# Performance work log

Hardware: AMD Instinct MI355X
Metric: run time of the kernel (lower is better)

## Reference

```python
import jax, jax.numpy as jnp
import numpy as np
import math

D_MODEL = 1024
D_STATE = 16
D_CONV = 4
EXPAND = 2
D_INNER = EXPAND * D_MODEL  # 2048
DT_RANK = 64
B_SZ = 2
L_SEQ = 1024


def setup_inputs() -> dict:
    key = jax.random.key(0)
    ks = jax.random.split(key, 10)
    x = jax.random.normal(ks[0], (B_SZ, L_SEQ, D_MODEL), dtype=jnp.float32)
    in_proj_w = jax.random.normal(ks[1], (2 * D_INNER, D_MODEL), dtype=jnp.float32) * (1.0 / math.sqrt(D_MODEL))
    conv_w = jax.random.normal(ks[2], (D_INNER, 1, D_CONV), dtype=jnp.float32) * (1.0 / math.sqrt(D_CONV))
    conv_b = jax.random.normal(ks[3], (D_INNER,), dtype=jnp.float32) * 0.01
    x_proj_w = jax.random.normal(ks[4], (DT_RANK + 2 * D_STATE, D_INNER), dtype=jnp.float32) * (1.0 / math.sqrt(D_INNER))
    dt_init_std = DT_RANK ** (-0.5)
    dt_proj_w = jax.random.uniform(ks[5], (D_INNER, DT_RANK), dtype=jnp.float32, minval=-dt_init_std, maxval=dt_init_std)
    dt = jnp.exp(jax.random.uniform(ks[6], (D_INNER,), dtype=jnp.float32) * (math.log(0.1) - math.log(0.001)) + math.log(0.001))
    dt = jnp.clip(dt, 1e-4, None)
    dt_proj_b = dt + jnp.log(-jnp.expm1(-dt))
    A_log = jnp.log(jnp.tile(jnp.arange(1, D_STATE + 1, dtype=jnp.float32)[None, :], (D_INNER, 1)))
    D = jnp.ones((D_INNER,), dtype=jnp.float32)
    out_proj_w = jax.random.normal(ks[7], (D_MODEL, D_INNER), dtype=jnp.float32) * (1.0 / math.sqrt(D_INNER))
    return {"x": x, "in_proj_w": in_proj_w, "conv_w": conv_w, "conv_b": conv_b,
            "x_proj_w": x_proj_w, "dt_proj_w": dt_proj_w, "dt_proj_b": dt_proj_b,
            "A_log": A_log, "D": D, "out_proj_w": out_proj_w}


def _mamba_forward(x, in_proj_w, conv_w, conv_b, x_proj_w, dt_proj_w, dt_proj_b, A_log, D, out_proj_w):
    B, L, _ = x.shape
    # input projection -> x, z each [B, L, Di]
    xz = jnp.einsum('bld,ed->ble', x, in_proj_w)
    xs, z = jnp.split(xz, 2, axis=-1)
    # causal depthwise conv along L (torch pads K-1 both sides then trims -> left pad only)
    xc = jnp.transpose(xs, (0, 2, 1))  # [B, Di, L]
    xc = jax.lax.conv_general_dilated(
        xc, conv_w, window_strides=(1,), padding=[(D_CONV - 1, 0)],
        feature_group_count=D_INNER, dimension_numbers=('NCH', 'OIH', 'NCH'))
    xc = xc + conv_b[None, :, None]
    xs = jnp.transpose(xc, (0, 2, 1))  # [B, L, Di]
    xs = jax.nn.silu(xs)
    # SSM parameters
    A = -jnp.exp(A_log)  # [Di, N]
    dbc = jnp.einsum('bld,ed->ble', xs, x_proj_w)
    delta_r = dbc[..., :DT_RANK]
    Bm = dbc[..., DT_RANK:DT_RANK + D_STATE]       # [B, L, N]
    Cm = dbc[..., DT_RANK + D_STATE:]              # [B, L, N]
    delta = jnp.einsum('blr,dr->bld', delta_r, dt_proj_w)
    delta = jax.nn.softplus(delta + dt_proj_b)     # [B, L, Di]
    # selective scan: h_t = exp(delta*A)*h_{t-1} + delta*B*x
    dA = jnp.exp(delta[..., None] * A)                          # [B, L, Di, N]
    dBx = (delta * xs)[..., None] * Bm[:, :, None, :]           # [B, L, Di, N]
    dA_t = jnp.moveaxis(dA, 1, 0)    # [L, B, Di, N]
    dBx_t = jnp.moveaxis(dBx, 1, 0)
    C_t = jnp.moveaxis(Cm, 1, 0)     # [L, B, N]
    h0 = jnp.zeros((B, D_INNER, D_STATE), dtype=xs.dtype)

    def step(h, inp):
        da, bx, c = inp
        h = da * h + bx
        y = jnp.einsum('bdn,bn->bd', h, c)
        return h, y

    _, ys = jax.lax.scan(step, h0, (dA_t, dBx_t, C_t))
    y = jnp.moveaxis(ys, 0, 1)       # [B, L, Di]
    y = y + D * xs
    # gating and output projection
    out = y * jax.nn.silu(z)
    return jnp.einsum('bld,od->blo', out, out_proj_w)


def reference(x, in_proj_w, conv_w, conv_b, x_proj_w, dt_proj_w, dt_proj_b, A_log, D, out_proj_w):
    return _mamba_forward(x, in_proj_w, conv_w, conv_b, x_proj_w, dt_proj_w, dt_proj_b, A_log, D, out_proj_w)
```

## Files before the change

kernel.cpp:

```cpp
#include <hip/hip_runtime.h>
#include <hip/hip_bf16.h>

typedef __attribute__((ext_vector_type(8))) short short8;
typedef __attribute__((ext_vector_type(4))) float f32x4;
typedef __hip_bfloat16 bf16;

#define D_MODEL 1024
#define D_INNER 2048
#define DT_RANK 64
#define D_STATE 16
#define B_SZ 2
#define L_SEQ 1024
#define NSEG 32
#define SL 32

__device__ __forceinline__ float b2f(bf16 x){ return __bfloat162float(x); }
__device__ __forceinline__ bf16  f2b(float x){ return __float2bfloat16(x); }

__device__ __forceinline__ void cvt_store8(bf16* dst, const float* s){
  union { short8 v; bf16 e[8]; } u;
  #pragma unroll
  for (int i = 0; i < 8; i++) u.e[i] = f2b(s[i]);
  *(short8*)dst = u.v;
}

__device__ __forceinline__ void gl_lds16(const bf16* g, bf16* l){
  __builtin_amdgcn_global_load_lds((const __attribute__((address_space(1))) unsigned int*)g,
                                   (__attribute__((address_space(3))) unsigned int*)l, 16, 0, 0);
}

__global__ __launch_bounds__(256) void cvt5_k(const float* s0, bf16* d0, int c0,
                                              const float* s1, bf16* d1, int c1,
                                              const float* s2, bf16* d2, int c2,
                                              const float* s3, bf16* d3, int c3,
                                              const float* s4, bf16* d4, int c4)
{
  int i = blockIdx.x * 256 + threadIdx.x;
  const float* s; bf16* d; int off;
  if      (i < c0) { s = s0; d = d0; off = i; }
  else if (i < c1) { s = s1; d = d1; off = i - c0; }
  else if (i < c2) { s = s2; d = d2; off = i - c1; }
  else if (i < c3) { s = s3; d = d3; off = i - c2; }
  else if (i < c4) { s = s4; d = d4; off = i - c3; }
  else return;
  float b[8];
  *(float4*)&b[0] = *(const float4*)(s + (size_t)off * 8);
  *(float4*)&b[4] = *(const float4*)(s + (size_t)off * 8 + 4);
  cvt_store8(d + (size_t)off * 8, b);
}

template<int MODE, int JT>
__global__ __launch_bounds__(256) void gemm_glds(const bf16* __restrict__ A,
                                                 const bf16* __restrict__ B,
                                                 void* __restrict__ Cout,
                                                 int M, int N, int K)
{
  constexpr int BN = JT * 32;
  constexpr int BI = BN / 64;
  __shared__ bf16 As[128 * 32];
  __shared__ bf16 Bs[BN * 32];

  const int gx = gridDim.x;
  const int nwg = gx * gridDim.y;
  const int flat = blockIdx.y * gx + blockIdx.x;
  const int swz = (flat & 7) * (nwg >> 3) + (flat >> 3);
  const int bm = (swz / gx) * 128, bn = (swz % gx) * BN;

  const int tid  = threadIdx.x;
  const int lane = tid & 63, wave = tid >> 6;
  const int wm = (wave & 1) * 64, wn = (wave >> 1) * (JT * 16);
  const int r = lane & 15, q = lane >> 4;

  const bf16* asrc[2];
  #pragma unroll
  for (int i = 0; i < 2; i++) {
    int c = i * 256 + tid;
    asrc[i] = A + (size_t)(bm + (c >> 2)) * K + (c & 3) * 8;
  }
  const bf16* bsrc[BI];
  #pragma unroll
  for (int i = 0; i < BI; i++) {
    int c = i * 256 + tid;
    bsrc[i] = B + (size_t)(bn + (c >> 2)) * K + (c & 3) * 8;
  }

  f32x4 acc[4][JT];
  #pragma unroll
  for (int i = 0; i < 4; i++)
    #pragma unroll
    for (int j = 0; j < JT; j++) acc[i][j] = (f32x4){0.f,0.f,0.f,0.f};

  for (int k0 = 0; k0 < K; k0 += 32) {
    #pragma unroll
    for (int i = 0; i < 2; i++)
      gl_lds16(asrc[i] + k0, &As[(i * 256 + tid) * 8]);
    #pragma unroll
    for (int i = 0; i < BI; i++)
      gl_lds16(bsrc[i] + k0, &Bs[(i * 256 + tid) * 8]);
    __syncthreads();
    short8 af[4], bfr[JT];
    #pragma unroll
    for (int i = 0; i < 4; i++)  af[i]  = *(const short8*)&As[(wm + i*16 + r) * 32 + q*8];
    #pragma unroll
    for (int j = 0; j < JT; j++) bfr[j] = *(const short8*)&Bs[(wn + j*16 + r) * 32 + q*8];
    #pragma unroll
    for (int j = 0; j < JT; j++)
      #pragma unroll
      for (int i = 0; i < 4; i++)
        acc[i][j] = __builtin_amdgcn_mfma_f32_16x16x32_bf16(af[i], bfr[j], acc[i][j], 0, 0, 0);
    __syncthreads();
  }

  #pragma unroll
  for (int i = 0; i < 4; i++)
    #pragma unroll
    for (int j = 0; j < JT; j++)
      #pragma unroll
      for (int t = 0; t < 4; t++) {
        int row = bm + wm + i*16 + q*4 + t;
        int col = bn + wn + j*16 + r;
        float v = acc[i][j][t];
        if (MODE == 0) ((float*)Cout)[(size_t)row * N + col] = v;
        else           ((bf16*)Cout)[(size_t)row * N + col] = f2b(v);
      }
}

__global__ __launch_bounds__(256) void gemm_dt(const bf16* __restrict__ A,
                                               const bf16* __restrict__ W,
                                               float* __restrict__ Cout,
                                               const float* __restrict__ bias,
                                               int M, int N)
{
  __shared__ __align__(16) float stg[4][16][68];
  const int lane = threadIdx.x & 63, wave = threadIdx.x >> 6;
  const int ntg  = N >> 6;
  const int task = blockIdx.x * 4 + wave;
  const int mt   = task / ntg;
  const int ng   = task - mt * ntg;
  const int r = lane & 15, q = lane >> 4;

  const bf16* pa = A + (size_t)(mt*16 + r) * DT_RANK + q*8;
  short8 a0 = *(const short8*)pa;
  short8 a1 = *(const short8*)(pa + 32);

  #pragma unroll
  for (int j = 0; j < 4; j++) {
    const bf16* pb = W + (size_t)(ng*64 + j*16 + r) * DT_RANK + q*8;
    short8 b0 = *(const short8*)pb;
    short8 b1 = *(const short8*)(pb + 32);
    f32x4 c = {0.f,0.f,0.f,0.f};
    c = __builtin_amdgcn_mfma_f32_16x16x32_bf16(a0, b0, c, 0, 0, 0);
    c = __builtin_amdgcn_mfma_f32_16x16x32_bf16(a1, b1, c, 0, 0, 0);
    float bv = bias[ng*64 + j*16 + r];
    #pragma unroll
    for (int t = 0; t < 4; t++) {
      float xv = c[t] + bv;
      float sp = (xv > 20.f) ? xv : log1pf(__expf(xv));
      stg[wave][q*4 + t][j*16 + r] = sp;
    }
  }
  {
    int row = lane >> 2, q4 = lane & 3;
    const float* src = &stg[wave][row][q4 * 16];
    float4 w0 = *(const float4*)(src);
    float4 w1 = *(const float4*)(src + 4);
    float4 w2 = *(const float4*)(src + 8);
    float4 w3 = *(const float4*)(src + 12);
    float* gdst = Cout + (size_t)(mt*16 + row) * N + ng*64 + q4*16;
    *(float4*)(gdst)      = w0;
    *(float4*)(gdst + 4)  = w1;
    *(float4*)(gdst + 8)  = w2;
    *(float4*)(gdst + 12) = w3;
  }
}

__global__ __launch_bounds__(256) void gemm_xproj(const bf16* __restrict__ A,
                                                  const bf16* __restrict__ W,
                                                  float* __restrict__ dbc,
                                                  bf16* __restrict__ dr)
{
  const int K = D_INNER;
  const int lane = threadIdx.x & 63, wave = threadIdx.x >> 6;
  const int mt = blockIdx.y * 4 + wave;
  const int nt = blockIdx.x;
  const int r = lane & 15, q = lane >> 4;
  const bf16* pa = A + (size_t)(mt*16 + r) * K + q*8;
  const bf16* pb = W + (size_t)(nt*16 + r) * K + q*8;
  f32x4 a0 = {0.f,0.f,0.f,0.f}, a1 = a0, a2 = a0, a3 = a0;
  for (int k0 = 0; k0 < K; k0 += 128) {
    short8 x0 = *(const short8*)(pa + k0);
    short8 w0 = *(const short8*)(pb + k0);
    short8 x1 = *(const short8*)(pa + k0 + 32);
    short8 w1 = *(const short8*)(pb + k0 + 32);
    short8 x2 = *(const short8*)(pa + k0 + 64);
    short8 w2 = *(const short8*)(pb + k0 + 64);
    short8 x3 = *(const short8*)(pa + k0 + 96);
    short8 w3 = *(const short8*)(pb + k0 + 96);
    a0 = __builtin_amdgcn_mfma_f32_16x16x32_bf16(x0, w0, a0, 0, 0, 0);
    a1 = __builtin_amdgcn_mfma_f32_16x16x32_bf16(x1, w1, a1, 0, 0, 0);
    a2 = __builtin_amdgcn_mfma_f32_16x16x32_bf16(x2, w2, a2, 0, 0, 0);
    a3 = __builtin_amdgcn_mfma_f32_16x16x32_bf16(x3, w3, a3, 0, 0, 0);
  }
  f32x4 acc = (a0 + a1) + (a2 + a3);
  #pragma unroll
  for (int t = 0; t < 4; t++) {
    int row = mt*16 + q*4 + t;
    int col = nt*16 + r;
    dbc[(size_t)row * 96 + col] = acc[t];
    if (col < DT_RANK) dr[(size_t)row * DT_RANK + col] = f2b(acc[t]);
  }
}

__global__ __launch_bounds__(256) void conv_silu_k(const bf16* __restrict__ xz,
                                                   const float* __restrict__ cw,
                                                   const float* __restrict__ cb,
                                                   bf16* __restrict__ xs_b)
{
  int idx = blockIdx.x * 256 + threadIdx.x;
  int dg = idx & (D_INNER/8 - 1);
  int bl = idx >> 8;
  int l  = bl & (L_SEQ - 1);
  int d0 = dg * 8;
  const float4* cw4 = (const float4*)cw;
  float4 w[8];
  #pragma unroll
  for (int i = 0; i < 8; i++) w[i] = cw4[d0 + i];
  float acc[8];
  #pragma unroll
  for (int i = 0; i < 8; i++) acc[i] = cb[d0 + i];
  #pragma unroll
  for (int j = 0; j < 4; ++j) {
    int lp = l - 3 + j;
    if (lp >= 0) {
      short8 v = *(const short8*)(xz + (size_t)(bl - 3 + j) * (2*D_INNER) + d0);
      #pragma unroll
      for (int i = 0; i < 8; i++)
        acc[i] += ((const float*)&w[i])[j] * b2f(((const bf16*)&v)[i]);
    }
  }
  float o[8];
  #pragma unroll
  for (int i = 0; i < 8; i++) o[i] = acc[i] / (1.f + __expf(-acc[i]));
  cvt_store8(xs_b + (size_t)idx * 8, o);
}

__device__ __forceinline__ bool an_is_int(const float* An){
  bool f = true;
  #pragma unroll
  for (int n = 0; n < 16; n++) f = f & (fabsf(An[n] + (float)(n+1)) < 1e-3f);
  return f;
}

__global__ __launch_bounds__(256) void scan_pass1(const float* __restrict__ delta,
                                                  const bf16* __restrict__ xs,
                                                  const float* __restrict__ dbc,
                                                  const float* __restrict__ A_log,
                                                  float* __restrict__ hseg,
                                                  float* __restrict__ Stot)
{
  __shared__ float bcs[SL][32];
  const int d   = blockIdx.x * 256 + threadIdx.x;
  const int seg = blockIdx.y, b = blockIdx.z;
  for (int i = threadIdx.x; i < SL*32; i += 256) {
    int l = i >> 5, c = i & 31;
    bcs[l][c] = dbc[((size_t)b*L_SEQ + seg*SL + l)*96 + DT_RANK + c];
  }
  __syncthreads();
  float An[16], h[16];
  #pragma unroll
  for (int n = 0; n < 16; n++) { An[n] = -__expf(A_log[d*16 + n]); h[n] = 0.f; }
  float S = 0.f;
  if (an_is_int(An)) {
    for (int li = 0; li < SL; ++li) {
      size_t bl = (size_t)b * L_SEQ + seg*SL + li;
      float dv = delta[bl*D_INNER + d];
      float xv = b2f(xs[bl*D_INNER + d]);
      S += dv;
      float dx = dv * xv;
      float q = __expf(-dv), w = 1.f;
      #pragma unroll
      for (int n = 0; n < 16; n++) {
        w *= q;
        h[n] = w * h[n] + dx * bcs[li][n];
      }
    }
  } else {
    for (int li = 0; li < SL; ++li) {
      size_t bl = (size_t)b * L_SEQ + seg*SL + li;
      float dv = delta[bl*D_INNER + d];
      float xv = b2f(xs[bl*D_INNER + d]);
      S += dv;
      float dx = dv * xv;
      #pragma unroll
      for (int n = 0; n < 16; n++)
        h[n] = __expf(dv * An[n]) * h[n] + dx * bcs[li][n];
    }
  }
  float* hp = hseg + (((size_t)seg*B_SZ + b)*D_INNER + d) * 16;
  #pragma unroll
  for (int n = 0; n < 16; n++) hp[n] = h[n];
  Stot[((size_t)seg*B_SZ + b)*D_INNER + d] = S;
}

__global__ __launch_bounds__(256) void scan_combine(const float* __restrict__ Stot,
                                                    float* __restrict__ hseg,
                                                    const float* __restrict__ A_log)
{
  int idx = blockIdx.x * 256 + threadIdx.x;
  int n = idx & 15;
  int d = (idx >> 4) & (D_INNER - 1);
  int b = idx >> 15;
  float An = -__expf(A_log[d*16 + n]);
  float H = 0.f;
  for (int s = 0; s < NSEG; s++) {
    size_t base = ((size_t)s*B_SZ + b)*D_INNER + d;
    float St   = Stot[base];
    float hloc = hseg[base*16 + n];
    hseg[base*16 + n] = H;
    H = __expf(An*St)*H + hloc;
  }
}

__global__ __launch_bounds__(256) void scan_pass3(const float* __restrict__ delta,
                                                  const bf16* __restrict__ xs,
                                                  const float* __restrict__ dbc,
                                                  const float* __restrict__ A_log,
                                                  const float* __restrict__ hseg,
                                                  const bf16* __restrict__ xz,
                                                  const float* __restrict__ Dw,
                                                  bf16* __restrict__ outin)
{
  __shared__ float bcs[SL][32];
  const int d   = blockIdx.x * 256 + threadIdx.x;
  const int seg = blockIdx.y, b = blockIdx.z;
  for (int i = threadIdx.x; i < SL*32; i += 256) {
    int l = i >> 5, c = i & 31;
    bcs[l][c] = dbc[((size_t)b*L_SEQ + seg*SL + l)*96 + DT_RANK + c];
  }
  __syncthreads();
  float An[16], h[16];
  const float* hp = hseg + (((size_t)seg*B_SZ + b)*D_INNER + d) * 16;
  #pragma unroll
  for (int n = 0; n < 16; n++) { An[n] = -__expf(A_log[d*16 + n]); h[n] = hp[n]; }
  const float Dv = Dw[d];
  if (an_is_int(An)) {
    for (int li = 0; li < SL; ++li) {
      size_t bl = (size_t)b * L_SEQ + seg*SL + li;
      float dv = delta[bl*D_INNER + d];
      float xv = b2f(xs[bl*D_INNER + d]);
      float dx = dv * xv;
      float q = __expf(-dv), w = 1.f;
      float y = 0.f;
      #pragma unroll
      for (int n = 0; n < 16; n++) {
        w *= q;
        h[n] = w * h[n] + dx * bcs[li][n];
        y   += h[n] * bcs[li][16 + n];
      }
      y += Dv * xv;
      float z = b2f(xz[bl*(size_t)(2*D_INNER) + D_INNER + d]);
      float g = z / (1.f + __expf(-z));
      outin[bl*D_INNER + d] = f2b(y * g);
    }
  } else {
    for (int li = 0; li < SL; ++li) {
      size_t bl = (size_t)b * L_SEQ + seg*SL + li;
      float dv = delta[bl*D_INNER + d];
      float xv = b2f(xs[bl*D_INNER + d]);
      float dx = dv * xv;
      float y = 0.f;
      #pragma unroll
      for (int n = 0; n < 16; n++) {
        h[n] = __expf(dv * An[n]) * h[n] + dx * bcs[li][n];
        y   += h[n] * bcs[li][16 + n];
      }
      y += Dv * xv;
      float z = b2f(xz[bl*(size_t)(2*D_INNER) + D_INNER + d]);
      float g = z / (1.f + __expf(-z));
      outin[bl*D_INNER + d] = f2b(y * g);
    }
  }
}

extern "C" void kernel_launch(void* const* d_in, const int* in_sizes, int n_in,
                              void* d_out, int out_size, void* d_ws, size_t ws_size,
                              hipStream_t stream)
{
  const float* x      = (const float*)d_in[0];
  const float* in_w   = (const float*)d_in[1];
  const float* conv_w = (const float*)d_in[2];
  const float* conv_b = (const float*)d_in[3];
  const float* xp_w   = (const float*)d_in[4];
  const float* dt_w   = (const float*)d_in[5];
  const float* dt_b   = (const float*)d_in[6];
  const float* A_log  = (const float*)d_in[7];
  const float* Dw     = (const float*)d_in[8];
  const float* out_w  = (const float*)d_in[9];
  float* out = (float*)d_out;

  char* p = (char*)d_ws;
  bf16*  xz    = (bf16*)p;  p += (size_t)B_SZ*L_SEQ*2*D_INNER*2;
  bf16*  xs_b  = (bf16*)p;  p += (size_t)B_SZ*L_SEQ*D_INNER*2;
  float* dbc   = (float*)p; p += (size_t)B_SZ*L_SEQ*96*4;
  bf16*  dr    = (bf16*)p;  p += (size_t)B_SZ*L_SEQ*DT_RANK*2;
  float* delta = (float*)p; p += (size_t)B_SZ*L_SEQ*D_INNER*4;
  float* Stot  = (float*)p; p += (size_t)NSEG*B_SZ*D_INNER*4;
  bf16*  outin = (bf16*)p;  p += (size_t)B_SZ*L_SEQ*D_INNER*2;
  bf16*  xp_wb = (bf16*)p;  p += (size_t)(DT_RANK+2*D_STATE)*D_INNER*2;
  bf16*  dt_wb = (bf16*)p;  p += (size_t)D_INNER*DT_RANK*2;
  bf16*  ow_b  = (bf16*)p;  p += (size_t)D_MODEL*D_INNER*2;
  char* u = p;
  bf16*  xb    = (bf16*)u;
  bf16*  in_wb = (bf16*)(u + (size_t)B_SZ*L_SEQ*D_MODEL*2);
  float* hseg  = (float*)u;
  p += (size_t)B_SZ*L_SEQ*(D_MODEL + 2*D_INNER)*2;

  const int M = B_SZ * L_SEQ;

  cvt5_k<<<4256, 256, 0, stream>>>(x, xb, 262144,
                                   in_w, in_wb, 786432,
                                   xp_w, xp_wb, 811008,
                                   dt_w, dt_wb, 827392,
                                   out_w, ow_b, 1089536);
  gemm_glds<2,2><<<dim3(2*D_INNER/64, M/128), 256, 0, stream>>>(xb, in_wb, xz, M, 2*D_INNER, D_MODEL);
  conv_silu_k<<<(M*D_INNER/8)/256, 256, 0, stream>>>(xz, conv_w, conv_b, xs_b);
  gemm_xproj<<<dim3(6, M/64), 256, 0, stream>>>(xs_b, xp_wb, dbc, dr);
  gemm_dt<<<(M/16)*(D_INNER/64)/4, 256, 0, stream>>>(dr, dt_wb, delta, dt_b, M, D_INNER);
  scan_pass1<<<dim3(D_INNER/256, NSEG, B_SZ), 256, 0, stream>>>(delta, xs_b, dbc, A_log, hseg, Stot);
  scan_combine<<<(B_SZ*D_INNER*16)/256, 256, 0, stream>>>(Stot, hseg, A_log);
  scan_pass3<<<dim3(D_INNER/256, NSEG, B_SZ), 256, 0, stream>>>(delta, xs_b, dbc, A_log, hseg, xz, Dw, outin);
  gemm_glds<0,2><<<dim3(D_MODEL/64, M/128), 256, 0, stream>>>(outin, ow_b, out, M, D_MODEL, D_INNER);
}
```

Before: 255.3 us.

## Fuse conv, projections and scan stages into one cooperative persistent kernel

Replaces six separate launches (conv+silu, x_proj GEMM, dt GEMM with softplus, scan pass1, segment combine, scan pass3) with a single cooperative kernel of 512 blocks separated by grid-wide syncs. The intent is to eliminate inter-kernel launch gaps and tail effects between these short stages. In exchange each stage runs with a fixed 512-block grid, some stages leave blocks idle, and grid.sync adds its own barrier cost; shared memory is reused across stages.

New measurement: 592.1 us. +131.9%, slower.

```diff
diff --git a/kernel.cpp b/kernel.cpp
--- a/kernel.cpp
+++ b/kernel.cpp
@@ -1,5 +1,8 @@
 #include <hip/hip_runtime.h>
 #include <hip/hip_bf16.h>
+#include <hip/hip_cooperative_groups.h>
+
+namespace cg = cooperative_groups;
 
 typedef __attribute__((ext_vector_type(8))) short short8;
 typedef __attribute__((ext_vector_type(4))) float f32x4;
@@ -125,125 +128,6 @@
       }
 }
 
-__global__ __launch_bounds__(256) void gemm_dt(const bf16* __restrict__ A,
-                                               const bf16* __restrict__ W,
-                                               float* __restrict__ Cout,
-                                               const float* __restrict__ bias,
-                                               int M, int N)
-{
-  __shared__ __align__(16) float stg[4][16][68];
-  const int lane = threadIdx.x & 63, wave = threadIdx.x >> 6;
-  const int ntg  = N >> 6;
-  const int task = blockIdx.x * 4 + wave;
-  const int mt   = task / ntg;
-  const int ng   = task - mt * ntg;
-  const int r = lane & 15, q = lane >> 4;
-
-  const bf16* pa = A + (size_t)(mt*16 + r) * DT_RANK + q*8;
-  short8 a0 = *(const short8*)pa;
-  short8 a1 = *(const short8*)(pa + 32);
-
-  #pragma unroll
-  for (int j = 0; j < 4; j++) {
-    const bf16* pb = W + (size_t)(ng*64 + j*16 + r) * DT_RANK + q*8;
-    short8 b0 = *(const short8*)pb;
-    short8 b1 = *(const short8*)(pb + 32);
-    f32x4 c = {0.f,0.f,0.f,0.f};
-    c = __builtin_amdgcn_mfma_f32_16x16x32_bf16(a0, b0, c, 0, 0, 0);
-    c = __builtin_amdgcn_mfma_f32_16x16x32_bf16(a1, b1, c, 0, 0, 0);
-    float bv = bias[ng*64 + j*16 + r];
-    #pragma unroll
-    for (int t = 0; t < 4; t++) {
-      float xv = c[t] + bv;
-      float sp = (xv > 20.f) ? xv : log1pf(__expf(xv));
-      stg[wave][q*4 + t][j*16 + r] = sp;
-    }
-  }
-  {
-    int row = lane >> 2, q4 = lane & 3;
-    const float* src = &stg[wave][row][q4 * 16];
-    float4 w0 = *(const float4*)(src);
-    float4 w1 = *(const float4*)(src + 4);
-    float4 w2 = *(const float4*)(src + 8);
-    float4 w3 = *(const float4*)(src + 12);
-    float* gdst = Cout + (size_t)(mt*16 + row) * N + ng*64 + q4*16;
-    *(float4*)(gdst)      = w0;
-    *(float4*)(gdst + 4)  = w1;
-    *(float4*)(gdst + 8)  = w2;
-    *(float4*)(gdst + 12) = w3;
-  }
-}
-
-__global__ __launch_bounds__(256) void gemm_xproj(const bf16* __restrict__ A,
-                                                  const bf16* __restrict__ W,
-                                                  float* __restrict__ dbc,
-                                                  bf16* __restrict__ dr)
-{
-  const int K = D_INNER;
-  const int lane = threadIdx.x & 63, wave = threadIdx.x >> 6;
-  const int mt = blockIdx.y * 4 + wave;
-  const int nt = blockIdx.x;
-  const int r = lane & 15, q = lane >> 4;
-  const bf16* pa = A + (size_t)(mt*16 + r) * K + q*8;
-  const bf16* pb = W + (size_t)(nt*16 + r) * K + q*8;
-  f32x4 a0 = {0.f,0.f,0.f,0.f}, a1 = a0, a2 = a0, a3 = a0;
-  for (int k0 = 0; k0 < K; k0 += 128) {
-    short8 x0 = *(const short8*)(pa + k0);
-    short8 w0 = *(const short8*)(pb + k0);
-    short8 x1 = *(const short8*)(pa + k0 + 32);
-    short8 w1 = *(const short8*)(pb + k0 + 32);
-    short8 x2 = *(const short8*)(pa + k0 + 64);
-    short8 w2 = *(const short8*)(pb + k0 + 64);
-    short8 x3 = *(const short8*)(pa + k0 + 96);
-    short8 w3 = *(const short8*)(pb + k0 + 96);
-    a0 = __builtin_amdgcn_mfma_f32_16x16x32_bf16(x0, w0, a0, 0, 0, 0);
-    a1 = __builtin_amdgcn_mfma_f32_16x16x32_bf16(x1, w1, a1, 0, 0, 0);
-    a2 = __builtin_amdgcn_mfma_f32_16x16x32_bf16(x2, w2, a2, 0, 0, 0);
-    a3 = __builtin_amdgcn_mfma_f32_16x16x32_bf16(x3, w3, a3, 0, 0, 0);
-  }
-  f32x4 acc = (a0 + a1) + (a2 + a3);
-  #pragma unroll
-  for (int t = 0; t < 4; t++) {
-    int row = mt*16 + q*4 + t;
-    int col = nt*16 + r;
-    dbc[(size_t)row * 96 + col] = acc[t];
-    if (col < DT_RANK) dr[(size_t)row * DT_RANK + col] = f2b(acc[t]);
-  }
-}
-
-__global__ __launch_bounds__(256) void conv_silu_k(const bf16* __restrict__ xz,
-                                                   const float* __restrict__ cw,
-                                                   const float* __restrict__ cb,
-                                                   bf16* __restrict__ xs_b)
-{
-  int idx = blockIdx.x * 256 + threadIdx.x;
-  int dg = idx & (D_INNER/8 - 1);
-  int bl = idx >> 8;
-  int l  = bl & (L_SEQ - 1);
-  int d0 = dg * 8;
-  const float4* cw4 = (const float4*)cw;
-  float4 w[8];
-  #pragma unroll
-  for (int i = 0; i < 8; i++) w[i] = cw4[d0 + i];
-  float acc[8];
-  #pragma unroll
-  for (int i = 0; i < 8; i++) acc[i] = cb[d0 + i];
-  #pragma unroll
-  for (int j = 0; j < 4; ++j) {
-    int lp = l - 3 + j;
-    if (lp >= 0) {
-      short8 v = *(const short8*)(xz + (size_t)(bl - 3 + j) * (2*D_INNER) + d0);
-      #pragma unroll
-      for (int i = 0; i < 8; i++)
-        acc[i] += ((const float*)&w[i])[j] * b2f(((const bf16*)&v)[i]);
-    }
-  }
-  float o[8];
-  #pragma unroll
-  for (int i = 0; i < 8; i++) o[i] = acc[i] / (1.f + __expf(-acc[i]));
-  cvt_store8(xs_b + (size_t)idx * 8, o);
-}
-
 __device__ __forceinline__ bool an_is_int(const float* An){
   bool f = true;
   #pragma unroll
@@ -251,133 +135,234 @@
   return f;
 }
 
-__global__ __launch_bounds__(256) void scan_pass1(const float* __restrict__ delta,
-                                                  const bf16* __restrict__ xs,
-                                                  const float* __restrict__ dbc,
-                                                  const float* __restrict__ A_log,
-                                                  float* __restrict__ hseg,
-                                                  float* __restrict__ Stot)
+__global__ __launch_bounds__(256) void mega_k(
+    const bf16* __restrict__ xz, const float* __restrict__ cw,
+    const float* __restrict__ cb, bf16* __restrict__ xs_b,
+    const bf16* __restrict__ xp_wb, float* __restrict__ dbc,
+    bf16* __restrict__ dr, const bf16* __restrict__ dt_wb,
+    const float* __restrict__ dt_b, float* __restrict__ delta,
+    const float* __restrict__ A_log, float* __restrict__ hseg,
+    float* __restrict__ Stot, const float* __restrict__ Dw,
+    bf16* __restrict__ outin)
 {
-  __shared__ float bcs[SL][32];
-  const int d   = blockIdx.x * 256 + threadIdx.x;
-  const int seg = blockIdx.y, b = blockIdx.z;
-  for (int i = threadIdx.x; i < SL*32; i += 256) {
-    int l = i >> 5, c = i & 31;
-    bcs[l][c] = dbc[((size_t)b*L_SEQ + seg*SL + l)*96 + DT_RANK + c];
-  }
-  __syncthreads();
-  float An[16], h[16];
-  #pragma unroll
-  for (int n = 0; n < 16; n++) { An[n] = -__expf(A_log[d*16 + n]); h[n] = 0.f; }
-  float S = 0.f;
-  if (an_is_int(An)) {
-    for (int li = 0; li < SL; ++li) {
-      size_t bl = (size_t)b * L_SEQ + seg*SL + li;
-      float dv = delta[bl*D_INNER + d];
-      float xv = b2f(xs[bl*D_INNER + d]);
-      S += dv;
-      float dx = dv * xv;
-      float q = __expf(-dv), w = 1.f;
+  cg::grid_group grid = cg::this_grid();
+  const int bid  = blockIdx.x;
+  const int tid  = threadIdx.x;
+  const int lane = tid & 63, wave = tid >> 6;
+  const int gw   = bid * 4 + wave;
+
+  __shared__ __align__(16) char smem[4 * 16 * 68 * 4];
+
+  for (int u = bid; u < (B_SZ*L_SEQ*D_INNER/8)/256; u += 512) {
+    int idx = u * 256 + tid;
+    int dg = idx & (D_INNER/8 - 1);
+    int bl = idx >> 8;
+    int l  = bl & (L_SEQ - 1);
+    int d0 = dg * 8;
+    const float4* cw4 = (const float4*)cw;
+    float4 w[8];
+    #pragma unroll
+    for (int i = 0; i < 8; i++) w[i] = cw4[d0 + i];
+    float acc[8];
+    #pragma unroll
+    for (int i = 0; i < 8; i++) acc[i] = cb[d0 + i];
+    #pragma unroll
+    for (int j = 0; j < 4; ++j) {
+      int lp = l - 3 + j;
+      if (lp >= 0) {
+        short8 v = *(const short8*)(xz + (size_t)(bl - 3 + j) * (2*D_INNER) + d0);
+        #pragma unroll
+        for (int i = 0; i < 8; i++)
+          acc[i] += ((const float*)&w[i])[j] * b2f(((const bf16*)&v)[i]);
+      }
+    }
+    float o[8];
+    #pragma unroll
+    for (int i = 0; i < 8; i++) o[i] = acc[i] / (1.f + __expf(-acc[i]));
+    cvt_store8(xs_b + (size_t)idx * 8, o);
+  }
+  grid.sync();
+
+  if (gw < 768) {
+    const int K = D_INNER;
+    const int mt = gw / 6, nt = gw - mt * 6;
+    const int r = lane & 15, q = lane >> 4;
+    const bf16* pa = xs_b + (size_t)(mt*16 + r) * K + q*8;
+    const bf16* pb = xp_wb + (size_t)(nt*16 + r) * K + q*8;
+    f32x4 a0 = {0.f,0.f,0.f,0.f}, a1 = a0, a2 = a0, a3 = a0;
+    for (int k0 = 0; k0 < K; k0 += 128) {
+      short8 x0 = *(const short8*)(pa + k0);
+      short8 w0 = *(const short8*)(pb + k0);
+      short8 x1 = *(const short8*)(pa + k0 + 32);
+      short8 w1 = *(const short8*)(pb + k0 + 32);
+      short8 x2 = *(const short8*)(pa + k0 + 64);
+      short8 w2 = *(const short8*)(pb + k0 + 64);
+      short8 x3 = *(const short8*)(pa + k0 + 96);
+      short8 w3 = *(const short8*)(pb + k0 + 96);
+      a0 = __builtin_amdgcn_mfma_f32_16x16x32_bf16(x0, w0, a0, 0, 0, 0);
+      a1 = __builtin_amdgcn_mfma_f32_16x16x32_bf16(x1, w1, a1, 0, 0, 0);
+      a2 = __builtin_amdgcn_mfma_f32_16x16x32_bf16(x2, w2, a2, 0, 0, 0);
+      a3 = __builtin_amdgcn_mfma_f32_16x16x32_bf16(x3, w3, a3, 0, 0, 0);
+    }
+    f32x4 acc = (a0 + a1) + (a2 + a3);
+    #pragma unroll
+    for (int t = 0; t < 4; t++) {
+      int row = mt*16 + q*4 + t;
+      int col = nt*16 + r;
+      dbc[(size_t)row * 96 + col] = acc[t];
+      if (col < DT_RANK) dr[(size_t)row * DT_RANK + col] = f2b(acc[t]);
+    }
+  }
+  grid.sync();
+
+  {
+    const int N = D_INNER;
+    float (*stg)[68] = (float(*)[68])(smem + wave * 16*68*4);
+    const int r = lane & 15, q = lane >> 4;
+    for (int t = gw; t < 4096; t += 2048) {
+      int mt = t >> 5, ng = t & 31;
+      const bf16* pa = dr + (size_t)(mt*16 + r) * DT_RANK + q*8;
+      short8 a0 = *(const short8*)pa;
+      short8 a1 = *(const short8*)(pa + 32);
       #pragma unroll
-      for (int n = 0; n < 16; n++) {
-        w *= q;
-        h[n] = w * h[n] + dx * bcs[li][n];
-      }
-    }
-  } else {
-    for (int li = 0; li < SL; ++li) {
-      size_t bl = (size_t)b * L_SEQ + seg*SL + li;
-      float dv = delta[bl*D_INNER + d];
-      float xv = b2f(xs[bl*D_INNER + d]);
-      S += dv;
-      float dx = dv * xv;
-      #pragma unroll
-      for (int n = 0; n < 16; n++)
-        h[n] = __expf(dv * An[n]) * h[n] + dx * bcs[li][n];
-    }
-  }
-  float* hp = hseg + (((size_t)seg*B_SZ + b)*D_INNER + d) * 16;
-  #pragma unroll
-  for (int n = 0; n < 16; n++) hp[n] = h[n];
-  Stot[((size_t)seg*B_SZ + b)*D_INNER + d] = S;
-}
-
-__global__ __launch_bounds__(256) void scan_combine(const float* __restrict__ Stot,
-                                                    float* __restrict__ hseg,
-                                                    const float* __restrict__ A_log)
-{
-  int idx = blockIdx.x * 256 + threadIdx.x;
-  int n = idx & 15;
-  int d = (idx >> 4) & (D_INNER - 1);
-  int b = idx >> 15;
-  float An = -__expf(A_log[d*16 + n]);
-  float H = 0.f;
-  for (int s = 0; s < NSEG; s++) {
-    size_t base = ((size_t)s*B_SZ + b)*D_INNER + d;
-    float St   = Stot[base];
-    float hloc = hseg[base*16 + n];
-    hseg[base*16 + n] = H;
-    H = __expf(An*St)*H + hloc;
-  }
-}
-
-__global__ __launch_bounds__(256) void scan_pass3(const float* __restrict__ delta,
-                                                  const bf16* __restrict__ xs,
-                                                  const float* __restrict__ dbc,
-                                                  const float* __restrict__ A_log,
-                                                  const float* __restrict__ hseg,
-                                                  const bf16* __restrict__ xz,
-                                                  const float* __restrict__ Dw,
-                                                  bf16* __restrict__ outin)
-{
-  __shared__ float bcs[SL][32];
-  const int d   = blockIdx.x * 256 + threadIdx.x;
-  const int seg = blockIdx.y, b = blockIdx.z;
-  for (int i = threadIdx.x; i < SL*32; i += 256) {
-    int l = i >> 5, c = i & 31;
-    bcs[l][c] = dbc[((size_t)b*L_SEQ + seg*SL + l)*96 + DT_RANK + c];
-  }
-  __syncthreads();
-  float An[16], h[16];
-  const float* hp = hseg + (((size_t)seg*B_SZ + b)*D_INNER + d) * 16;
-  #pragma unroll
-  for (int n = 0; n < 16; n++) { An[n] = -__expf(A_log[d*16 + n]); h[n] = hp[n]; }
-  const float Dv = Dw[d];
-  if (an_is_int(An)) {
-    for (int li = 0; li < SL; ++li) {
-      size_t bl = (size_t)b * L_SEQ + seg*SL + li;
-      float dv = delta[bl*D_INNER + d];
-      float xv = b2f(xs[bl*D_INNER + d]);
-      float dx = dv * xv;
-      float q = __expf(-dv), w = 1.f;
-      float y = 0.f;
-      #pragma unroll
-      for (int n = 0; n < 16; n++) {
-        w *= q;
-        h[n] = w * h[n] + dx * bcs[li][n];
-        y   += h[n] * bcs[li][16 + n];
-      }
-      y += Dv * xv;
-      float z = b2f(xz[bl*(size_t)(2*D_INNER) + D_INNER + d]);
-      float g = z / (1.f + __expf(-z));
-      outin[bl*D_INNER + d] = f2b(y * g);
-    }
-  } else {
-    for (int li = 0; li < SL; ++li) {
-      size_t bl = (size_t)b * L_SEQ + seg*SL + li;
-      float dv = delta[bl*D_INNER + d];
-      float xv = b2f(xs[bl*D_INNER + d]);
-      float dx = dv * xv;
-      float y = 0.f;
-      #pragma unroll
-      for (int n = 0; n < 16; n++) {
-        h[n] = __expf(dv * An[n]) * h[n] + dx * bcs[li][n];
-        y   += h[n] * bcs[li][16 + n];
-      }
-      y += Dv * xv;
-      float z = b2f(xz[bl*(size_t)(2*D_INNER) + D_INNER + d]);
-      float g = z / (1.f + __expf(-z));
-      outin[bl*D_INNER + d] = f2b(y * g);
+      for (int j = 0; j < 4; j++) {
+        const bf16* pb = dt_wb + (size_t)(ng*64 + j*16 + r) * DT_RANK + q*8;
+        short8 b0 = *(const short8*)pb;
+        short8 b1 = *(const short8*)(pb + 32);
+        f32x4 c = {0.f,0.f,0.f,0.f};
+        c = __builtin_amdgcn_mfma_f32_16x16x32_bf16(a0, b0, c, 0, 0, 0);
+        c = __builtin_amdgcn_mfma_f32_16x16x32_bf16(a1, b1, c, 0, 0, 0);
+        float bv = dt_b[ng*64 + j*16 + r];
+        #pragma unroll
+        for (int tt = 0; tt < 4; tt++) {
+          float xv = c[tt] + bv;
+          float sp = (xv > 20.f) ? xv : log1pf(__expf(xv));
+          stg[q*4 + tt][j*16 + r] = sp;
+        }
+      }
+      int row = lane >> 2, q4 = lane & 3;
+      const float* src = &stg[row][q4 * 16];
+      float4 w0 = *(const float4*)(src);
+      float4 w1 = *(const float4*)(src + 4);
+      float4 w2 = *(const float4*)(src + 8);
+      float4 w3 = *(const float4*)(src + 12);
+      float* gdst = delta + (size_t)(mt*16 + row) * N + ng*64 + q4*16;
+      *(float4*)(gdst)      = w0;
+      *(float4*)(gdst + 4)  = w1;
+      *(float4*)(gdst + 8)  = w2;
+      *(float4*)(gdst + 12) = w3;
+    }
+  }
+  grid.sync();
+
+  const int d   = (bid & 7) * 256 + tid;
+  const int seg = (bid >> 3) & 31;
+  const int b   = bid >> 8;
+  float (*bcs)[32] = (float(*)[32])smem;
+
+  {
+    __syncthreads();
+    for (int i = tid; i < SL*32; i += 256) {
+      int l = i >> 5, c = i & 31;
+      bcs[l][c] = dbc[((size_t)b*L_SEQ + seg*SL + l)*96 + DT_RANK + c];
+    }
+    __syncthreads();
+    float An[16], h[16];
+    #pragma unroll
+    for (int n = 0; n < 16; n++) { An[n] = -__expf(A_log[d*16 + n]); h[n] = 0.f; }
+    float S = 0.f;
+    if (an_is_int(An)) {
+      for (int li = 0; li < SL; ++li) {
+        size_t bl = (size_t)b * L_SEQ + seg*SL + li;
+        float dv = delta[bl*D_INNER + d];
+        float xv = b2f(xs_b[bl*D_INNER + d]);
+        S += dv;
+        float dx = dv * xv;
+        float qq = __expf(-dv), w = 1.f;
+        #pragma unroll
+        for (int n = 0; n < 16; n++) {
+          w *= qq;
+          h[n] = w * h[n] + dx * bcs[li][n];
+        }
+      }
+    } else {
+      for (int li = 0; li < SL; ++li) {
+        size_t bl = (size_t)b * L_SEQ + seg*SL + li;
+        float dv = delta[bl*D_INNER + d];
+        float xv = b2f(xs_b[bl*D_INNER + d]);
+        S += dv;
+        float dx = dv * xv;
+        #pragma unroll
+        for (int n = 0; n < 16; n++)
+          h[n] = __expf(dv * An[n]) * h[n] + dx * bcs[li][n];
+      }
+    }
+    float* hp = hseg + (((size_t)seg*B_SZ + b)*D_INNER + d) * 16;
+    #pragma unroll
+    for (int n = 0; n < 16; n++) hp[n] = h[n];
+    Stot[((size_t)seg*B_SZ + b)*D_INNER + d] = S;
+  }
+  grid.sync();
+
+  if (bid < 256) {
+    int idx = bid * 256 + tid;
+    int n  = idx & 15;
+    int dd = (idx >> 4) & (D_INNER - 1);
+    int bb = idx >> 15;
+    float An = -__expf(A_log[dd*16 + n]);
+    float H = 0.f;
+    for (int s = 0; s < NSEG; s++) {
+      size_t base = ((size_t)s*B_SZ + bb)*D_INNER + dd;
+      float St   = Stot[base];
+      float hloc = hseg[base*16 + n];
+      hseg[base*16 + n] = H;
+      H = __expf(An*St)*H + hloc;
+    }
+  }
+  grid.sync();
+
+  {
+    float An[16], h[16];
+    const float* hp = hseg + (((size_t)seg*B_SZ + b)*D_INNER + d) * 16;
+    #pragma unroll
+    for (int n = 0; n < 16; n++) { An[n] = -__expf(A_log[d*16 + n]); h[n] = hp[n]; }
+    const float Dv = Dw[d];
+    if (an_is_int(An)) {
+      for (int li = 0; li < SL; ++li) {
+        size_t bl = (size_t)b * L_SEQ + seg*SL + li;
+        float dv = delta[bl*D_INNER + d];
+        float xv = b2f(xs_b[bl*D_INNER + d]);
+        float dx = dv * xv;
+        float qq = __expf(-dv), w = 1.f;
+        float y = 0.f;
+        #pragma unroll
+        for (int n = 0; n < 16; n++) {
+          w *= qq;
+          h[n] = w * h[n] + dx * bcs[li][n];
+          y   += h[n] * bcs[li][16 + n];
+        }
+        y += Dv * xv;
+        float z = b2f(xz[bl*(size_t)(2*D_INNER) + D_INNER + d]);
+        float g = z / (1.f + __expf(-z));
+        outin[bl*D_INNER + d] = f2b(y * g);
+      }
+    } else {
+      for (int li = 0; li < SL; ++li) {
+        size_t bl = (size_t)b * L_SEQ + seg*SL + li;
+        float dv = delta[bl*D_INNER + d];
+        float xv = b2f(xs_b[bl*D_INNER + d]);
+        float dx = dv * xv;
+        float y = 0.f;
+        #pragma unroll
+        for (int n = 0; n < 16; n++) {
+          h[n] = __expf(dv * An[n]) * h[n] + dx * bcs[li][n];
+          y   += h[n] * bcs[li][16 + n];
+        }
+        y += Dv * xv;
+        float z = b2f(xz[bl*(size_t)(2*D_INNER) + D_INNER + d]);
+        float g = z / (1.f + __expf(-z));
+        outin[bl*D_INNER + d] = f2b(y * g);
+      }
     }
   }
 }
@@ -423,11 +408,15 @@
                                    dt_w, dt_wb, 827392,
                                    out_w, ow_b, 1089536);
   gemm_glds<2,2><<<dim3(2*D_INNER/64, M/128), 256, 0, stream>>>(xb, in_wb, xz, M, 2*D_INNER, D_MODEL);
-  conv_silu_k<<<(M*D_INNER/8)/256, 256, 0, stream>>>(xz, conv_w, conv_b, xs_b);
-  gemm_xproj<<<dim3(6, M/64), 256, 0, stream>>>(xs_b, xp_wb, dbc, dr);
-  gemm_dt<<<(M/16)*(D_INNER/64)/4, 256, 0, stream>>>(dr, dt_wb, delta, dt_b, M, D_INNER);
-  scan_pass1<<<dim3(D_INNER/256, NSEG, B_SZ), 256, 0, stream>>>(delta, xs_b, dbc, A_log, hseg, Stot);
-  scan_combine<<<(B_SZ*D_INNER*16)/256, 256, 0, stream>>>(Stot, hseg, A_log);
-  scan_pass3<<<dim3(D_INNER/256, NSEG, B_SZ), 256, 0, stream>>>(delta, xs_b, dbc, A_log, hseg, xz, Dw, outin);
+  {
+    void* kargs[] = {
+      (void*)&xz, (void*)&conv_w, (void*)&conv_b, (void*)&xs_b,
+      (void*)&xp_wb, (void*)&dbc, (void*)&dr, (void*)&dt_wb,
+      (void*)&dt_b, (void*)&delta, (void*)&A_log, (void*)&hseg,
+      (void*)&Stot, (void*)&Dw, (void*)&outin
+    };
+    hipLaunchCooperativeKernel((const void*)mega_k, dim3(512), dim3(256),
+                               kargs, 0, stream);
+  }
   gemm_glds<0,2><<<dim3(D_MODEL/64, M/128), 256, 0, stream>>>(outin, ow_b, out, M, D_MODEL, D_INNER);
 }
```
